# Optimization experiments

Hardware: AMD Instinct MI355X
Metric: run time of the kernel (lower is better)

The kernel has to match this reference:

```python
import jax, jax.numpy as jnp
import numpy as np

N = 50000      # nodes in batched graph
E = 800000     # edges
IN_DIM = 16
HID = 64
NH = 4         # heads
G = 128        # graphs in batch
OUT_DIM = 32
NUM_LAYERS = 8
NEG_SLOPE = 0.2  # DGL GATv2Conv default


def setup_inputs() -> dict:
    key = jax.random.key(0)
    ks = jax.random.split(key, 12)
    feat = jax.random.normal(ks[0], (N, IN_DIM), dtype=jnp.float32)
    src = jax.random.randint(ks[1], (E,), 0, N, dtype=jnp.int32)
    dst = jax.random.randint(ks[2], (E,), 0, N, dtype=jnp.int32)
    graph_ids = jnp.sort(jax.random.randint(ks[3], (N,), 0, G, dtype=jnp.int32))
    is_root = jax.random.randint(ks[4], (N,), 0, 2, dtype=jnp.int32)
    s_in = 1.0 / np.sqrt(IN_DIM)
    s_h = 1.0 / np.sqrt(2 * HID)
    s_o = 1.0 / np.sqrt(HID)
    return {
        'feat': feat, 'src': src, 'dst': dst,
        'graph_ids': graph_ids, 'is_root': is_root,
        'W_in': jax.random.normal(ks[5], (IN_DIM, HID), jnp.float32) * s_in,
        'b_in': jnp.zeros((HID,), jnp.float32),
        'W_src': jax.random.normal(ks[6], (2 * HID, NH * HID), jnp.float32) * s_h,
        'b_src': jnp.zeros((NH * HID,), jnp.float32),
        'W_dst': jax.random.normal(ks[7], (2 * HID, NH * HID), jnp.float32) * s_h,
        'b_dst': jnp.zeros((NH * HID,), jnp.float32),
        'attn': jax.random.normal(ks[8], (NH, HID), jnp.float32) * s_o,
        'W_out': jax.random.normal(ks[9], (HID, OUT_DIM), jnp.float32) * s_o,
        'b_out': jnp.zeros((OUT_DIM,), jnp.float32),
    }


def reference(feat, src, dst, graph_ids, is_root,
              W_in, b_in, W_src, b_src, W_dst, b_dst, attn, W_out, b_out):
    h0 = feat @ W_in + b_in                       # [N, HID]
    h = h0
    for _ in range(NUM_LAYERS):
        x = jnp.concatenate([h, h0], axis=1)      # [N, 2*HID]
        fs = (x @ W_src + b_src).reshape(-1, NH, HID)  # [N, NH, HID]
        fd = (x @ W_dst + b_dst).reshape(-1, NH, HID)
        # per-edge GATv2 attention logits
        e = jax.nn.leaky_relu(fs[src] + fd[dst], NEG_SLOPE)   # [E, NH, HID]
        s = jnp.einsum('ehd,hd->eh', e, attn)                 # [E, NH]
        # segment softmax over incoming edges of each dst node
        m = jax.ops.segment_max(s, dst, num_segments=N)       # [N, NH]
        a = jnp.exp(s - m[dst])
        denom = jax.ops.segment_sum(a, dst, num_segments=N)
        alpha = a / denom[dst]                                # [E, NH]
        # weighted aggregation of source features
        agg = jax.ops.segment_sum(alpha[:, :, None] * fs[src], dst,
                                  num_segments=N)             # [N, NH, HID]
        h = jnp.tanh(agg).sum(axis=1)                         # [N, HID]
    # root-weighted readout per graph
    hg = jax.ops.segment_sum(h * is_root.astype(h.dtype)[:, None],
                             graph_ids, num_segments=G)       # [G, HID]
    return hg @ W_out + b_out                                 # [G, OUT_DIM]
```

## Files before the change

kernel.cpp:

```cpp
#include <hip/hip_runtime.h>
#include <math.h>

#define N_NODES 50000
#define N_EDGES 800000
#define IN_DIM  16
#define HID     64
#define NH      4
#define NGRAPH  128
#define OUT_DIM 32
#define NUM_LAYERS 8
#define NEG_SLOPE 0.2f

#define SCAN_BLOCKS ((N_NODES + 255) / 256)

typedef unsigned short u16;
typedef unsigned char  u8;
typedef _Float16 h2   __attribute__((ext_vector_type(2)));
typedef _Float16 f16x8 __attribute__((ext_vector_type(8)));
typedef float f32x2 __attribute__((ext_vector_type(2)));
typedef __attribute__((ext_vector_type(4))) float f32x4;

static __device__ __forceinline__ u16 f2h(float f) {
    _Float16 h = (_Float16)f; u16 r; __builtin_memcpy(&r, &h, 2); return r;
}
static __device__ __forceinline__ float h2f_lo(unsigned w) {
    _Float16 h; u16 u = (u16)w; __builtin_memcpy(&h, &u, 2); return (float)h;
}
static __device__ __forceinline__ h2 shfl_h2(h2 v, int mask) {
    int i; __builtin_memcpy(&i, &v, 4); i = __shfl_xor(i, mask);
    h2 r; __builtin_memcpy(&r, &i, 4); return r;
}
static __device__ __forceinline__ h2 bcast_h2(float f) {
    _Float16 h = (_Float16)f; h2 r; r[0] = h; r[1] = h; return r;
}

#define DPP_XOR1(x) __uint_as_float((unsigned)__builtin_amdgcn_update_dpp(0, (int)__float_as_uint(x), 0xB1, 0xF, 0xF, true))
#define DPP_XOR2(x) __uint_as_float((unsigned)__builtin_amdgcn_update_dpp(0, (int)__float_as_uint(x), 0x4E, 0xF, 0xF, true))


__global__ void k_build_wpack(const float* __restrict__ Wsrc, const float* __restrict__ bsrc,
                              const float* __restrict__ Wdst, const float* __restrict__ bdst,
                              const float* __restrict__ attn,
                              u16* __restrict__ Wpack, float* __restrict__ bcat,
                              u16* __restrict__ an_h) {
    int tid = blockIdx.x * 256 + threadIdx.x;
    int i = tid & 7;
    int l = (tid >> 3) & 63;
    int rest = tid >> 9;
    int kt = rest & 3;
    int nt = rest >> 2;
    int k = kt * 32 + (l >> 4) * 8 + i;
    int col = nt * 16 + (l & 15);
    float v = (col < 256) ? Wsrc[k * 256 + col] : Wdst[k * 256 + (col - 256)];
    Wpack[tid] = f2h(v);
    if (tid < 512) bcat[tid] = (tid < 256) ? bsrc[tid] : bdst[tid - 256];
    if (tid < 256) an_h[tid] = f2h(attn[tid] * 1.44269504f);
}

__global__ void k_hist(const int* __restrict__ dst, int* __restrict__ deg) {
    int e = blockIdx.x * 256 + threadIdx.x;
    if (e < N_EDGES) atomicAdd(&deg[dst[e]], 1);
}

__global__ void k_blocksum(const int* __restrict__ deg, int* __restrict__ bsum) {
    __shared__ int sm[256];
    int i = blockIdx.x * 256 + threadIdx.x;
    sm[threadIdx.x] = (i < N_NODES) ? deg[i] : 0;
    __syncthreads();
    for (int s = 128; s > 0; s >>= 1) {
        if (threadIdx.x < s) sm[threadIdx.x] += sm[threadIdx.x + s];
        __syncthreads();
    }
    if (threadIdx.x == 0) bsum[blockIdx.x] = sm[0];
}

__global__ void k_scanbsum(int* __restrict__ bsum) {
    if (threadIdx.x == 0 && blockIdx.x == 0) {
        int acc = 0;
        for (int b = 0; b < SCAN_BLOCKS; b++) { int t = bsum[b]; bsum[b] = acc; acc += t; }
    }
}

__global__ void k_rowptr(const int* __restrict__ deg, const int* __restrict__ bsum,
                         int* __restrict__ row_ptr) {
    __shared__ int sm[256];
    int i = blockIdx.x * 256 + threadIdx.x;
    int v = (i < N_NODES) ? deg[i] : 0;
    sm[threadIdx.x] = v;
    __syncthreads();
    for (int s = 1; s < 256; s <<= 1) {
        int t = (threadIdx.x >= (unsigned)s) ? sm[threadIdx.x - s] : 0;
        __syncthreads();
        sm[threadIdx.x] += t;
        __syncthreads();
    }
    if (i < N_NODES) row_ptr[i] = bsum[blockIdx.x] + sm[threadIdx.x] - v;
}

__global__ void k_scatter(const int* __restrict__ src, const int* __restrict__ dst,
                          const int* __restrict__ row_ptr, int* __restrict__ cursor,
                          int* __restrict__ csr_src) {
    int e = blockIdx.x * 256 + threadIdx.x;
    if (e < N_EDGES) {
        int d = dst[e];
        int pos = atomicAdd(&cursor[d], 1);
        csr_src[row_ptr[d] + pos] = src[e];
    }
}

__global__ __launch_bounds__(256) void k_in_gemm(const float* __restrict__ feat,
                                                 const float* __restrict__ W,
                                                 const float* __restrict__ b,
                                                 u16* __restrict__ h0h) {
    __shared__ float sW[IN_DIM * HID];
    __shared__ float sb[HID];
    int t = threadIdx.x;
    for (int i = t; i < IN_DIM * HID; i += 256) sW[i] = W[i];
    if (t < HID) sb[t] = b[t];
    __syncthreads();
    int wid = (blockIdx.x * 256 + t) >> 6;
    int lane = t & 63;
    const float* f = feat + wid * IN_DIM;
    float acc = sb[lane];
    #pragma unroll
    for (int k = 0; k < IN_DIM; k++) acc += f[k] * sW[k * HID + lane];
    h0h[wid * HID + lane] = f2h(acc);
}


#define ST_STRIDE 152
__global__ __launch_bounds__(256) void k_gemm_mfma(const u16* __restrict__ hb,
                                                   const u16* __restrict__ h0b,
                                                   const u16* __restrict__ Wpack,
                                                   const float* __restrict__ bcat,
                                                   u16* __restrict__ fsh,
                                                   u16* __restrict__ fdh) {
    __shared__ u16 sW[16384];
    __shared__ u16 sStage[4][2432];
    int tid = threadIdx.x;
    int g  = blockIdx.x & 3;
    int tb = blockIdx.x >> 2;
    int l = tid & 63, w = tid >> 6;
    int lr = l & 15, lg = l >> 4;

    {
        const f16x8* src = (const f16x8*)(Wpack + g * 16384);
        f16x8* dst = (f16x8*)sW;
        #pragma unroll
        for (int it = 0; it < 8; it++) dst[it * 256 + tid] = src[it * 256 + tid];
    }
    __syncthreads();

    size_t row0 = (size_t)(tb * 4 + w) * 16;
    if (row0 >= N_NODES) return;

    f32x4 acc[8];
    #pragma unroll
    for (int nt = 0; nt < 8; nt++) acc[nt] = (f32x4){0.f, 0.f, 0.f, 0.f};

    #pragma unroll
    for (int kt = 0; kt < 4; kt++) {
        const u16* A = (kt < 2) ? hb : h0b;
        f16x8 a = *(const f16x8*)(A + (row0 + lr) * HID + (kt & 1) * 32 + lg * 8);
        #pragma unroll
        for (int nt = 0; nt < 8; nt++) {
            f16x8 bfr = *(const f16x8*)(sW + nt * 2048 + kt * 512 + l * 8);
            acc[nt] = __builtin_amdgcn_mfma_f32_16x16x32_f16(a, bfr, acc[nt], 0, 0, 0);
        }
    }

    u16* myst = sStage[w];
    #pragma unroll
    for (int nt = 0; nt < 8; nt++) {
        float bv = bcat[g * 128 + nt * 16 + lr];
        #pragma unroll
        for (int j = 0; j < 4; j++)
            myst[(lg * 4 + j) * ST_STRIDE + nt * 16 + lr] = f2h(acc[nt][j] + bv);
    }
    u16* dsth = (g < 2) ? fsh : fdh;
    int colh = (g & 1) * 128;
    #pragma unroll
    for (int j = 0; j < 4; j++) {
        int rloc = j * 4 + lg;
        f16x8 v = *(const f16x8*)(myst + rloc * ST_STRIDE + lr * 8);
        *(f16x8*)(dsth + (row0 + rloc) * 256 + colh + lr * 8) = v;
    }
}

__global__ __launch_bounds__(256) void k_edge(const u16* __restrict__ fsh,
                                              const u16* __restrict__ fdh,
                                              const u16* __restrict__ an_h,
                                              const int* __restrict__ row_ptr,
                                              const int* __restrict__ deg,
                                              const int* __restrict__ csr_src,
                                              u16* __restrict__ h) {
    int wid = (blockIdx.x * 256 + threadIdx.x) >> 6;
    int lane = threadIdx.x & 63;
    int g  = lane >> 4;
    int ll = lane & 15;
    const size_t ebase = (size_t)ll * 16;

    h2 an[8], fdhv[8];
    {
        const uint4* ap = (const uint4*)(an_h + ebase);
        uint4 a0 = ap[0], a1 = ap[1];
        unsigned aw[8] = {a0.x, a0.y, a0.z, a0.w, a1.x, a1.y, a1.z, a1.w};
        __builtin_memcpy(an, aw, 32);
        const uint4* fp = (const uint4*)(fdh + (size_t)wid * 256 + ebase);
        uint4 b0 = fp[0], b1 = fp[1];
        unsigned fw[8] = {b0.x, b0.y, b0.z, b0.w, b1.x, b1.y, b1.z, b1.w};
        __builtin_memcpy(fdhv, fw, 32);
    }
    const h2 slope2 = {(_Float16)NEG_SLOPE, (_Float16)NEG_SLOPE};

    float m = -3.0e38f, denom = 0.f;
    h2 agg[8];
    #pragma unroll
    for (int q = 0; q < 8; q++) agg[q] = (h2){(_Float16)0.f, (_Float16)0.f};

    int r0 = row_ptr[wid], dg = deg[wid];

    uint4 A0 = {0,0,0,0}, A1 = {0,0,0,0};
    if (g < dg) {
        int s = csr_src[r0 + g];
        const uint4* P = (const uint4*)(fsh + (size_t)s * 256 + ebase);
        A0 = P[0]; A1 = P[1];
    }

    for (int i = g; i < dg; i += 4) {
        int inext = i + 4;
        bool hN = inext < dg;
        int sN = csr_src[r0 + (hN ? inext : i)];
        const uint4* PN = (const uint4*)(fsh + (size_t)sN * 256 + ebase);
        uint4 B0 = PN[0], B1 = PN[1];

        h2 f[8];
        {
            unsigned fw[8] = {A0.x, A0.y, A0.z, A0.w, A1.x, A1.y, A1.z, A1.w};
            __builtin_memcpy(f, fw, 32);
        }
        float p0 = 0.f, p1 = 0.f;
        #pragma unroll
        for (int q = 0; q < 8; q += 2) {
            h2 e0 = f[q]   + fdhv[q];
            h2 e1 = f[q+1] + fdhv[q+1];
            h2 l0 = __builtin_elementwise_max(e0, e0 * slope2);
            h2 l1 = __builtin_elementwise_max(e1, e1 * slope2);
            p0 = __builtin_amdgcn_fdot2(l0, an[q],   p0, false);
            p1 = __builtin_amdgcn_fdot2(l1, an[q+1], p1, false);
        }
        float p = p0 + p1;
        p += DPP_XOR1(p);
        p += DPP_XOR2(p);

        float c;
        if (__builtin_expect(p > m + 4.f, 0)) {
            float rs = exp2f(m - p);
            h2 rs2 = bcast_h2(rs);
            #pragma unroll
            for (int q = 0; q < 8; q++) agg[q] = agg[q] * rs2;
            denom *= rs;
            m = p;
            c = 1.f;
        } else {
            c = exp2f(p - m);
        }
        h2 c2 = bcast_h2(c);
        #pragma unroll
        for (int q = 0; q < 8; q++) agg[q] = agg[q] + f[q] * c2;
        denom += c;

        A0 = B0; A1 = B1;
    }

    {
        float mm = fmaxf(m, __shfl_xor(m, 16));
        mm = fmaxf(mm, __shfl_xor(mm, 32));
        float sc = exp2f(m - mm);
        denom *= sc;
        h2 sc2 = bcast_h2(sc);
        #pragma unroll
        for (int q = 0; q < 8; q++) agg[q] = agg[q] * sc2;
        denom += __shfl_xor(denom, 16);
        denom += __shfl_xor(denom, 32);
        #pragma unroll
        for (int q = 0; q < 8; q++) {
            agg[q] = agg[q] + shfl_h2(agg[q], 16);
            agg[q] = agg[q] + shfl_h2(agg[q], 32);
        }
    }

    float inv = denom > 0.f ? __builtin_amdgcn_rcpf(denom) : 0.f;
    float inv2 = inv * 2.885390082f;

    h2 x0 = (g & 2) ? ((g & 1) ? agg[6] : agg[4]) : ((g & 1) ? agg[2] : agg[0]);
    h2 x1 = (g & 2) ? ((g & 1) ? agg[7] : agg[5]) : ((g & 1) ? agg[3] : agg[1]);
    float t[4] = {(float)x0[0], (float)x0[1], (float)x1[0], (float)x1[1]};
    #pragma unroll
    for (int j = 0; j < 4; j++) {
        float E = exp2f(t[j] * inv2);
        float r = __builtin_amdgcn_rcpf(E + 1.f);
        float v = fmaf(-2.f, r, 1.f);
        v += __shfl_xor(v, 4);
        v += __shfl_xor(v, 8);
        t[j] = v;
    }
    if (ll < 4) {
        uint2 o;
        o.x = (unsigned)f2h(t[0]) | ((unsigned)f2h(t[1]) << 16);
        o.y = (unsigned)f2h(t[2]) | ((unsigned)f2h(t[3]) << 16);
        *(uint2*)(h + (size_t)wid * 64 + ll * 16 + g * 4) = o;
    }
}


__global__ __launch_bounds__(256) void k_readout(const u16* __restrict__ h,
                                                 const int* __restrict__ graph_ids,
                                                 const int* __restrict__ is_root,
                                                 float* __restrict__ hg) {
    int wid = (blockIdx.x * 256 + threadIdx.x) >> 6;
    int lane = threadIdx.x & 63;
    if (is_root[wid]) {
        int g = graph_ids[wid];
        atomicAdd(&hg[g * HID + lane], h2f_lo(h[(size_t)wid * HID + lane]));
    }
}

__global__ void k_out_gemm(const float* __restrict__ hg, const float* __restrict__ W,
                           const float* __restrict__ b, float* __restrict__ out) {
    int i = blockIdx.x * 256 + threadIdx.x;
    if (i >= NGRAPH * OUT_DIM) return;
    int g = i >> 5, o = i & 31;
    float acc = b[o];
    #pragma unroll
    for (int k = 0; k < HID; k++) acc += hg[g * HID + k] * W[k * OUT_DIM + o];
    out[i] = acc;
}


extern "C" void kernel_launch(void* const* d_in, const int* in_sizes, int n_in,
                              void* d_out, int out_size, void* d_ws, size_t ws_size,
                              hipStream_t stream) {
    const float* feat      = (const float*)d_in[0];
    const int*   src       = (const int*)d_in[1];
    const int*   dst       = (const int*)d_in[2];
    const int*   graph_ids = (const int*)d_in[3];
    const int*   is_root   = (const int*)d_in[4];
    const float* W_in      = (const float*)d_in[5];
    const float* b_in      = (const float*)d_in[6];
    const float* W_src     = (const float*)d_in[7];
    const float* b_src     = (const float*)d_in[8];
    const float* W_dst     = (const float*)d_in[9];
    const float* b_dst     = (const float*)d_in[10];
    const float* attn      = (const float*)d_in[11];
    const float* W_out     = (const float*)d_in[12];
    const float* b_out     = (const float*)d_in[13];
    float* out = (float*)d_out;

    char* base = (char*)d_ws;
    size_t off = 0;
    auto carve = [&](size_t bytes) -> char* {
        char* p = base + off;
        off = (off + bytes + 255) & ~(size_t)255;
        return p;
    };
    u16*   h0b     = (u16*)carve((size_t)N_NODES * HID * 2);
    u16*   hb      = (u16*)carve((size_t)N_NODES * HID * 2);
    u16*   fsh     = (u16*)carve((size_t)N_NODES * 256 * 2);
    u16*   fdh     = (u16*)carve((size_t)N_NODES * 256 * 2);
    u16*   Wpack   = (u16*)carve(128 * 512 * 2);
    float* bcat    = (float*)carve(512 * 4);
    u16*   an_h    = (u16*)carve(256 * 2);
    int*   csr_src = (int*)carve((size_t)N_EDGES * 4);
    int*   row_ptr = (int*)carve((size_t)N_NODES * 4);
    int*   bsum    = (int*)carve(SCAN_BLOCKS * 4);
    char*  zero0   = carve(0);
    int*   deg     = (int*)carve((size_t)N_NODES * 4);
    int*   cursor  = (int*)carve((size_t)N_NODES * 4);
    float* hg      = (float*)carve((size_t)NGRAPH * HID * 4);
    char*  zero1   = base + off;
    if (off > ws_size) return;

    (void)hipMemsetAsync(zero0, 0, (size_t)(zero1 - zero0), stream);

    k_build_wpack<<<256, 256, 0, stream>>>(W_src, b_src, W_dst, b_dst, attn, Wpack, bcat, an_h);
    k_hist<<<(N_EDGES + 255) / 256, 256, 0, stream>>>(dst, deg);
    k_blocksum<<<SCAN_BLOCKS, 256, 0, stream>>>(deg, bsum);
    k_scanbsum<<<1, 64, 0, stream>>>(bsum);
    k_rowptr<<<SCAN_BLOCKS, 256, 0, stream>>>(deg, bsum, row_ptr);
    k_scatter<<<(N_EDGES + 255) / 256, 256, 0, stream>>>(src, dst, row_ptr, cursor, csr_src);

    k_in_gemm<<<N_NODES / 4, 256, 0, stream>>>(feat, W_in, b_in, h0b);

    const int gemm_grid = ((N_NODES / 16 + 3) / 4) * 4;
    for (int layer = 0; layer < NUM_LAYERS; layer++) {
        const u16* hcur = (layer == 0) ? h0b : hb;
        k_gemm_mfma<<<gemm_grid, 256, 0, stream>>>(hcur, h0b, Wpack, bcat, fsh, fdh);
        k_edge<<<N_NODES / 4, 256, 0, stream>>>(fsh, fdh, an_h, row_ptr, deg, csr_src, hb);
    }

    k_readout<<<N_NODES / 4, 256, 0, stream>>>(hb, graph_ids, is_root, hg);
    k_out_gemm<<<(NGRAPH * OUT_DIM + 255) / 256, 256, 0, stream>>>(hg, W_out, b_out, out);
}
```

Before: 862.7 us.

## Fuse all stages into one persistent cooperative kernel with grid syncs

```diff
diff --git a/kernel.cpp b/kernel.cpp
--- a/kernel.cpp
+++ b/kernel.cpp
@@ -1,5 +1,8 @@
 #include <hip/hip_runtime.h>
+#include <hip/hip_cooperative_groups.h>
 #include <math.h>
+
+namespace cg = cooperative_groups;
 
 #define N_NODES 50000
 #define N_EDGES 800000
@@ -12,12 +15,11 @@
 #define NEG_SLOPE 0.2f
 
 #define SCAN_BLOCKS ((N_NODES + 255) / 256)
+#define ST_STRIDE 152
 
 typedef unsigned short u16;
-typedef unsigned char  u8;
 typedef _Float16 h2   __attribute__((ext_vector_type(2)));
 typedef _Float16 f16x8 __attribute__((ext_vector_type(8)));
-typedef float f32x2 __attribute__((ext_vector_type(2)));
 typedef __attribute__((ext_vector_type(4))) float f32x4;
 
 static __device__ __forceinline__ u16 f2h(float f) {
@@ -37,325 +39,294 @@
 #define DPP_XOR1(x) __uint_as_float((unsigned)__builtin_amdgcn_update_dpp(0, (int)__float_as_uint(x), 0xB1, 0xF, 0xF, true))
 #define DPP_XOR2(x) __uint_as_float((unsigned)__builtin_amdgcn_update_dpp(0, (int)__float_as_uint(x), 0x4E, 0xF, 0xF, true))
 
-
-__global__ void k_build_wpack(const float* __restrict__ Wsrc, const float* __restrict__ bsrc,
-                              const float* __restrict__ Wdst, const float* __restrict__ bdst,
-                              const float* __restrict__ attn,
-                              u16* __restrict__ Wpack, float* __restrict__ bcat,
-                              u16* __restrict__ an_h) {
-    int tid = blockIdx.x * 256 + threadIdx.x;
-    int i = tid & 7;
-    int l = (tid >> 3) & 63;
-    int rest = tid >> 9;
-    int kt = rest & 3;
-    int nt = rest >> 2;
-    int k = kt * 32 + (l >> 4) * 8 + i;
-    int col = nt * 16 + (l & 15);
-    float v = (col < 256) ? Wsrc[k * 256 + col] : Wdst[k * 256 + (col - 256)];
-    Wpack[tid] = f2h(v);
-    if (tid < 512) bcat[tid] = (tid < 256) ? bsrc[tid] : bdst[tid - 256];
-    if (tid < 256) an_h[tid] = f2h(attn[tid] * 1.44269504f);
-}
-
-__global__ void k_hist(const int* __restrict__ dst, int* __restrict__ deg) {
-    int e = blockIdx.x * 256 + threadIdx.x;
-    if (e < N_EDGES) atomicAdd(&deg[dst[e]], 1);
-}
-
-__global__ void k_blocksum(const int* __restrict__ deg, int* __restrict__ bsum) {
-    __shared__ int sm[256];
-    int i = blockIdx.x * 256 + threadIdx.x;
-    sm[threadIdx.x] = (i < N_NODES) ? deg[i] : 0;
+struct Params {
+    const float* feat; const int* src; const int* dst;
+    const int* graph_ids; const int* is_root;
+    const float* W_in; const float* b_in;
+    const float* W_src; const float* b_src;
+    const float* W_dst; const float* b_dst;
+    const float* attn; const float* W_out; const float* b_out;
+    float* out;
+    u16* h0b; u16* hb; u16* fsh; u16* fdh; u16* Wpack;
+    float* bcat; u16* an_h;
+    int* csr_src; int* row_ptr; int* bsum; int* deg; int* cursor;
+    float* hg;
+};
+
+__global__ __launch_bounds__(256, 4) void k_fused(Params P) {
+    cg::grid_group grid = cg::this_grid();
+    const int bid = blockIdx.x, nb = gridDim.x, tid = threadIdx.x;
+    const int gthread = bid * 256 + tid, nthreads = nb * 256;
+    const int l = tid & 63, w = tid >> 6;
+    const int lr = l & 15, lg = l >> 4;
+
+    __shared__ __align__(16) char smem_raw[19456];
+
+    for (int i = gthread; i < N_NODES; i += nthreads) { P.deg[i] = 0; P.cursor[i] = 0; }
+    for (int i = gthread; i < NGRAPH * HID; i += nthreads) P.hg[i] = 0.f;
+    for (int t = gthread; t < 65536; t += nthreads) {
+        int ii = t & 7;
+        int ll2 = (t >> 3) & 63;
+        int rest = t >> 9;
+        int kt = rest & 3;
+        int nt = rest >> 2;
+        int k = kt * 32 + (ll2 >> 4) * 8 + ii;
+        int col = nt * 16 + (ll2 & 15);
+        float v = (col < 256) ? P.W_src[k * 256 + col] : P.W_dst[k * 256 + (col - 256)];
+        P.Wpack[t] = f2h(v);
+        if (t < 512) P.bcat[t] = (t < 256) ? P.b_src[t] : P.b_dst[t - 256];
+        if (t < 256) P.an_h[t] = f2h(P.attn[t] * 1.44269504f);
+    }
+    grid.sync();
+
+    for (int e = gthread; e < N_EDGES; e += nthreads) atomicAdd(&P.deg[P.dst[e]], 1);
+    grid.sync();
+
+    int* sm = (int*)smem_raw;
+    if (bid < SCAN_BLOCKS) {
+        int i = bid * 256 + tid;
+        sm[tid] = (i < N_NODES) ? P.deg[i] : 0;
+        __syncthreads();
+        for (int s = 128; s > 0; s >>= 1) {
+            if (tid < s) sm[tid] += sm[tid + s];
+            __syncthreads();
+        }
+        if (tid == 0) P.bsum[bid] = sm[0];
+    }
+    grid.sync();
+
+    if (bid == 0 && tid == 0) {
+        int acc = 0;
+        for (int b = 0; b < SCAN_BLOCKS; b++) { int t2 = P.bsum[b]; P.bsum[b] = acc; acc += t2; }
+    }
+    grid.sync();
+
+    if (bid < SCAN_BLOCKS) {
+        int i = bid * 256 + tid;
+        int v = (i < N_NODES) ? P.deg[i] : 0;
+        sm[tid] = v;
+        __syncthreads();
+        for (int s = 1; s < 256; s <<= 1) {
+            int t2 = (tid >= s) ? sm[tid - s] : 0;
+            __syncthreads();
+            sm[tid] += t2;
+            __syncthreads();
+        }
+        if (i < N_NODES) P.row_ptr[i] = P.bsum[bid] + sm[tid] - v;
+    }
+    grid.sync();
+
+    for (int e = gthread; e < N_EDGES; e += nthreads) {
+        int d = P.dst[e];
+        int pos = atomicAdd(&P.cursor[d], 1);
+        P.csr_src[P.row_ptr[d] + pos] = P.src[e];
+    }
     __syncthreads();
-    for (int s = 128; s > 0; s >>= 1) {
-        if (threadIdx.x < s) sm[threadIdx.x] += sm[threadIdx.x + s];
-        __syncthreads();
-    }
-    if (threadIdx.x == 0) bsum[blockIdx.x] = sm[0];
-}
-
-__global__ void k_scanbsum(int* __restrict__ bsum) {
-    if (threadIdx.x == 0 && blockIdx.x == 0) {
-        int acc = 0;
-        for (int b = 0; b < SCAN_BLOCKS; b++) { int t = bsum[b]; bsum[b] = acc; acc += t; }
-    }
-}
-
-__global__ void k_rowptr(const int* __restrict__ deg, const int* __restrict__ bsum,
-                         int* __restrict__ row_ptr) {
-    __shared__ int sm[256];
-    int i = blockIdx.x * 256 + threadIdx.x;
-    int v = (i < N_NODES) ? deg[i] : 0;
-    sm[threadIdx.x] = v;
+    float* sWin = (float*)smem_raw;
+    float* sbin = sWin + 1024;
+    for (int i = tid; i < IN_DIM * HID; i += 256) sWin[i] = P.W_in[i];
+    if (tid < HID) sbin[tid] = P.b_in[tid];
     __syncthreads();
-    for (int s = 1; s < 256; s <<= 1) {
-        int t = (threadIdx.x >= (unsigned)s) ? sm[threadIdx.x - s] : 0;
-        __syncthreads();
-        sm[threadIdx.x] += t;
-        __syncthreads();
-    }
-    if (i < N_NODES) row_ptr[i] = bsum[blockIdx.x] + sm[threadIdx.x] - v;
-}
-
-__global__ void k_scatter(const int* __restrict__ src, const int* __restrict__ dst,
-                          const int* __restrict__ row_ptr, int* __restrict__ cursor,
-                          int* __restrict__ csr_src) {
-    int e = blockIdx.x * 256 + threadIdx.x;
-    if (e < N_EDGES) {
-        int d = dst[e];
-        int pos = atomicAdd(&cursor[d], 1);
-        csr_src[row_ptr[d] + pos] = src[e];
-    }
-}
-
-__global__ __launch_bounds__(256) void k_in_gemm(const float* __restrict__ feat,
-                                                 const float* __restrict__ W,
-                                                 const float* __restrict__ b,
-                                                 u16* __restrict__ h0h) {
-    __shared__ float sW[IN_DIM * HID];
-    __shared__ float sb[HID];
-    int t = threadIdx.x;
-    for (int i = t; i < IN_DIM * HID; i += 256) sW[i] = W[i];
-    if (t < HID) sb[t] = b[t];
-    __syncthreads();
-    int wid = (blockIdx.x * 256 + t) >> 6;
-    int lane = t & 63;
-    const float* f = feat + wid * IN_DIM;
-    float acc = sb[lane];
-    #pragma unroll
-    for (int k = 0; k < IN_DIM; k++) acc += f[k] * sW[k * HID + lane];
-    h0h[wid * HID + lane] = f2h(acc);
-}
-
-
-#define ST_STRIDE 152
-__global__ __launch_bounds__(256) void k_gemm_mfma(const u16* __restrict__ hb,
-                                                   const u16* __restrict__ h0b,
-                                                   const u16* __restrict__ Wpack,
-                                                   const float* __restrict__ bcat,
-                                                   u16* __restrict__ fsh,
-                                                   u16* __restrict__ fdh) {
-    __shared__ u16 sW[16384];
-    __shared__ u16 sStage[4][2432];
-    int tid = threadIdx.x;
-    int g  = blockIdx.x & 3;
-    int tb = blockIdx.x >> 2;
-    int l = tid & 63, w = tid >> 6;
-    int lr = l & 15, lg = l >> 4;
-
-    {
-        const f16x8* src = (const f16x8*)(Wpack + g * 16384);
-        f16x8* dst = (f16x8*)sW;
+    for (int v = bid; v < N_NODES / 4; v += nb) {
+        int node = v * 4 + w;
+        const float* f = P.feat + node * IN_DIM;
+        float acc = sbin[l];
         #pragma unroll
-        for (int it = 0; it < 8; it++) dst[it * 256 + tid] = src[it * 256 + tid];
-    }
-    __syncthreads();
-
-    size_t row0 = (size_t)(tb * 4 + w) * 16;
-    if (row0 >= N_NODES) return;
-
-    f32x4 acc[8];
-    #pragma unroll
-    for (int nt = 0; nt < 8; nt++) acc[nt] = (f32x4){0.f, 0.f, 0.f, 0.f};
-
-    #pragma unroll
-    for (int kt = 0; kt < 4; kt++) {
-        const u16* A = (kt < 2) ? hb : h0b;
-        f16x8 a = *(const f16x8*)(A + (row0 + lr) * HID + (kt & 1) * 32 + lg * 8);
+        for (int k = 0; k < IN_DIM; k++) acc += f[k] * sWin[k * HID + l];
+        P.h0b[node * HID + l] = f2h(acc);
+    }
+    grid.sync();
+
+    const int nbg = nb >> 2;
+    const int g = bid & 3;
+    const int myg = bid >> 2;
+    const u16* WpG = P.Wpack + g * 16384;
+    u16* sStage = (u16*)smem_raw;
+    const h2 slope2 = {(_Float16)NEG_SLOPE, (_Float16)NEG_SLOPE};
+
+    for (int layer = 0; layer < NUM_LAYERS; layer++) {
+        const u16* hcur = (layer == 0) ? P.h0b : P.hb;
+
+        for (int tb = myg; tb < (N_NODES / 16 + 3) / 4; tb += nbg) {
+            size_t row0 = (size_t)(tb * 4 + w) * 16;
+            if (row0 >= N_NODES) continue;
+            f32x4 acc[8];
+            #pragma unroll
+            for (int nt = 0; nt < 8; nt++) acc[nt] = (f32x4){0.f, 0.f, 0.f, 0.f};
+            #pragma unroll
+            for (int kt = 0; kt < 4; kt++) {
+                const u16* A = (kt < 2) ? hcur : P.h0b;
+                f16x8 a = *(const f16x8*)(A + (row0 + lr) * HID + (kt & 1) * 32 + lg * 8);
+                #pragma unroll
+                for (int nt = 0; nt < 8; nt++) {
+                    f16x8 bfr = *(const f16x8*)(WpG + nt * 2048 + kt * 512 + l * 8);
+                    acc[nt] = __builtin_amdgcn_mfma_f32_16x16x32_f16(a, bfr, acc[nt], 0, 0, 0);
+                }
+            }
+            u16* myst = sStage + w * 2432;
+            #pragma unroll
+            for (int nt = 0; nt < 8; nt++) {
+                float bv = P.bcat[g * 128 + nt * 16 + lr];
+                #pragma unroll
+                for (int j = 0; j < 4; j++)
+                    myst[(lg * 4 + j) * ST_STRIDE + nt * 16 + lr] = f2h(acc[nt][j] + bv);
+            }
+            u16* dsth = (g < 2) ? P.fsh : P.fdh;
+            int colh = (g & 1) * 128;
+            #pragma unroll
+            for (int j = 0; j < 4; j++) {
+                int rloc = j * 4 + lg;
+                f16x8 vv = *(const f16x8*)(myst + rloc * ST_STRIDE + lr * 8);
+                *(f16x8*)(dsth + (row0 + rloc) * 256 + colh + lr * 8) = vv;
+            }
+        }
+        grid.sync();
+
+        for (int v = bid; v < N_NODES / 4; v += nb) {
+            int wid = v * 4 + w;
+            int eg = lg;
+            int ll = lr;
+            const size_t ebase = (size_t)ll * 16;
+
+            h2 an[8], fdhv[8];
+            {
+                const uint4* ap = (const uint4*)(P.an_h + ebase);
+                uint4 a0 = ap[0], a1 = ap[1];
+                unsigned aw[8] = {a0.x, a0.y, a0.z, a0.w, a1.x, a1.y, a1.z, a1.w};
+                __builtin_memcpy(an, aw, 32);
+                const uint4* fp = (const uint4*)(P.fdh + (size_t)wid * 256 + ebase);
+                uint4 b0 = fp[0], b1 = fp[1];
+                unsigned fw[8] = {b0.x, b0.y, b0.z, b0.w, b1.x, b1.y, b1.z, b1.w};
+                __builtin_memcpy(fdhv, fw, 32);
+            }
+
+            float m = -3.0e38f, denom = 0.f;
+            h2 agg[8];
+            #pragma unroll
+            for (int q = 0; q < 8; q++) agg[q] = (h2){(_Float16)0.f, (_Float16)0.f};
+
+            int r0 = P.row_ptr[wid], dg = P.deg[wid];
+            for (int i = eg; i < dg; i += 4) {
+                int s = P.csr_src[r0 + i];
+                const uint4* Pr = (const uint4*)(P.fsh + (size_t)s * 256 + ebase);
+                uint4 A0 = Pr[0], A1 = Pr[1];
+                h2 f[8];
+                {
+                    unsigned fw[8] = {A0.x, A0.y, A0.z, A0.w, A1.x, A1.y, A1.z, A1.w};
+                    __builtin_memcpy(f, fw, 32);
+                }
+                float p0 = 0.f, p1 = 0.f;
+                #pragma unroll
+                for (int q = 0; q < 8; q += 2) {
+                    h2 e0 = f[q]   + fdhv[q];
+                    h2 e1 = f[q+1] + fdhv[q+1];
+                    h2 l0 = __builtin_elementwise_max(e0, e0 * slope2);
+                    h2 l1 = __builtin_elementwise_max(e1, e1 * slope2);
+                    p0 = __builtin_amdgcn_fdot2(l0, an[q],   p0, false);
+                    p1 = __builtin_amdgcn_fdot2(l1, an[q+1], p1, false);
+                }
+                float p = p0 + p1;
+                p += DPP_XOR1(p);
+                p += DPP_XOR2(p);
+
+                float c;
+                if (__builtin_expect(p > m + 4.f, 0)) {
+                    float rs = exp2f(m - p);
+                    h2 rs2 = bcast_h2(rs);
+                    #pragma unroll
+                    for (int q = 0; q < 8; q++) agg[q] = agg[q] * rs2;
+                    denom *= rs;
+                    m = p;
+                    c = 1.f;
+                } else {
+                    c = exp2f(p - m);
+                }
+                h2 c2 = bcast_h2(c);
+                #pragma unroll
+                for (int q = 0; q < 8; q++) agg[q] = agg[q] + f[q] * c2;
+                denom += c;
+            }
+
+            {
+                float mm = fmaxf(m, __shfl_xor(m, 16));
+                mm = fmaxf(mm, __shfl_xor(mm, 32));
+                float sc = exp2f(m - mm);
+                denom *= sc;
+                h2 sc2 = bcast_h2(sc);
+                #pragma unroll
+                for (int q = 0; q < 8; q++) agg[q] = agg[q] * sc2;
+                denom += __shfl_xor(denom, 16);
+                denom += __shfl_xor(denom, 32);
+                #pragma unroll
+                for (int q = 0; q < 8; q++) {
+                    agg[q] = agg[q] + shfl_h2(agg[q], 16);
+                    agg[q] = agg[q] + shfl_h2(agg[q], 32);
+                }
+            }
+
+            float inv = denom > 0.f ? __builtin_amdgcn_rcpf(denom) : 0.f;
+            float inv2 = inv * 2.885390082f;
+
+            h2 x0 = (eg & 2) ? ((eg & 1) ? agg[6] : agg[4]) : ((eg & 1) ? agg[2] : agg[0]);
+            h2 x1 = (eg & 2) ? ((eg & 1) ? agg[7] : agg[5]) : ((eg & 1) ? agg[3] : agg[1]);
+            float t[4] = {(float)x0[0], (float)x0[1], (float)x1[0], (float)x1[1]};
+            #pragma unroll
+            for (int j = 0; j < 4; j++) {
+                float E = exp2f(t[j] * inv2);
+                float r = __builtin_amdgcn_rcpf(E + 1.f);
+                float vv = fmaf(-2.f, r, 1.f);
+                vv += __shfl_xor(vv, 4);
+                vv += __shfl_xor(vv, 8);
+                t[j] = vv;
+            }
+            if (ll < 4) {
+                uint2 o;
+                o.x = (unsigned)f2h(t[0]) | ((unsigned)f2h(t[1]) << 16);
+                o.y = (unsigned)f2h(t[2]) | ((unsigned)f2h(t[3]) << 16);
+                *(uint2*)(P.hb + (size_t)wid * 64 + ll * 16 + eg * 4) = o;
+            }
+        }
+        grid.sync();
+    }
+
+    for (int v = bid; v < N_NODES / 4; v += nb) {
+        int wid = v * 4 + w;
+        if (P.is_root[wid]) {
+            int gg = P.graph_ids[wid];
+            atomicAdd(&P.hg[gg * HID + l], h2f_lo(P.hb[(size_t)wid * HID + l]));
+        }
+    }
+    grid.sync();
+
+    for (int i = gthread; i < NGRAPH * OUT_DIM; i += nthreads) {
+        int gg = i >> 5, o = i & 31;
+        float acc = P.b_out[o];
         #pragma unroll
-        for (int nt = 0; nt < 8; nt++) {
-            f16x8 bfr = *(const f16x8*)(sW + nt * 2048 + kt * 512 + l * 8);
-            acc[nt] = __builtin_amdgcn_mfma_f32_16x16x32_f16(a, bfr, acc[nt], 0, 0, 0);
-        }
-    }
-
-    u16* myst = sStage[w];
-    #pragma unroll
-    for (int nt = 0; nt < 8; nt++) {
-        float bv = bcat[g * 128 + nt * 16 + lr];
-        #pragma unroll
-        for (int j = 0; j < 4; j++)
-            myst[(lg * 4 + j) * ST_STRIDE + nt * 16 + lr] = f2h(acc[nt][j] + bv);
-    }
-    u16* dsth = (g < 2) ? fsh : fdh;
-    int colh = (g & 1) * 128;
-    #pragma unroll
-    for (int j = 0; j < 4; j++) {
-        int rloc = j * 4 + lg;
-        f16x8 v = *(const f16x8*)(myst + rloc * ST_STRIDE + lr * 8);
-        *(f16x8*)(dsth + (row0 + rloc) * 256 + colh + lr * 8) = v;
-    }
-}
-
-__global__ __launch_bounds__(256) void k_edge(const u16* __restrict__ fsh,
-                                              const u16* __restrict__ fdh,
-                                              const u16* __restrict__ an_h,
-                                              const int* __restrict__ row_ptr,
-                                              const int* __restrict__ deg,
-                                              const int* __restrict__ csr_src,
-                                              u16* __restrict__ h) {
-    int wid = (blockIdx.x * 256 + threadIdx.x) >> 6;
-    int lane = threadIdx.x & 63;
-    int g  = lane >> 4;
-    int ll = lane & 15;
-    const size_t ebase = (size_t)ll * 16;
-
-    h2 an[8], fdhv[8];
-    {
-        const uint4* ap = (const uint4*)(an_h + ebase);
-        uint4 a0 = ap[0], a1 = ap[1];
-        unsigned aw[8] = {a0.x, a0.y, a0.z, a0.w, a1.x, a1.y, a1.z, a1.w};
-        __builtin_memcpy(an, aw, 32);
-        const uint4* fp = (const uint4*)(fdh + (size_t)wid * 256 + ebase);
-        uint4 b0 = fp[0], b1 = fp[1];
-        unsigned fw[8] = {b0.x, b0.y, b0.z, b0.w, b1.x, b1.y, b1.z, b1.w};
-        __builtin_memcpy(fdhv, fw, 32);
-    }
-    const h2 slope2 = {(_Float16)NEG_SLOPE, (_Float16)NEG_SLOPE};
-
-    float m = -3.0e38f, denom = 0.f;
-    h2 agg[8];
-    #pragma unroll
-    for (int q = 0; q < 8; q++) agg[q] = (h2){(_Float16)0.f, (_Float16)0.f};
-
-    int r0 = row_ptr[wid], dg = deg[wid];
-
-    uint4 A0 = {0,0,0,0}, A1 = {0,0,0,0};
-    if (g < dg) {
-        int s = csr_src[r0 + g];
-        const uint4* P = (const uint4*)(fsh + (size_t)s * 256 + ebase);
-        A0 = P[0]; A1 = P[1];
-    }
-
-    for (int i = g; i < dg; i += 4) {
-        int inext = i + 4;
-        bool hN = inext < dg;
-        int sN = csr_src[r0 + (hN ? inext : i)];
-        const uint4* PN = (const uint4*)(fsh + (size_t)sN * 256 + ebase);
-        uint4 B0 = PN[0], B1 = PN[1];
-
-        h2 f[8];
-        {
-            unsigned fw[8] = {A0.x, A0.y, A0.z, A0.w, A1.x, A1.y, A1.z, A1.w};
-            __builtin_memcpy(f, fw, 32);
-        }
-        float p0 = 0.f, p1 = 0.f;
-        #pragma unroll
-        for (int q = 0; q < 8; q += 2) {
-            h2 e0 = f[q]   + fdhv[q];
-            h2 e1 = f[q+1] + fdhv[q+1];
-            h2 l0 = __builtin_elementwise_max(e0, e0 * slope2);
-            h2 l1 = __builtin_elementwise_max(e1, e1 * slope2);
-            p0 = __builtin_amdgcn_fdot2(l0, an[q],   p0, false);
-            p1 = __builtin_amdgcn_fdot2(l1, an[q+1], p1, false);
-        }
-        float p = p0 + p1;
-        p += DPP_XOR1(p);
-        p += DPP_XOR2(p);
-
-        float c;
-        if (__builtin_expect(p > m + 4.f, 0)) {
-            float rs = exp2f(m - p);
-            h2 rs2 = bcast_h2(rs);
-            #pragma unroll
-            for (int q = 0; q < 8; q++) agg[q] = agg[q] * rs2;
-            denom *= rs;
-            m = p;
-            c = 1.f;
-        } else {
-            c = exp2f(p - m);
-        }
-        h2 c2 = bcast_h2(c);
-        #pragma unroll
-        for (int q = 0; q < 8; q++) agg[q] = agg[q] + f[q] * c2;
-        denom += c;
-
-        A0 = B0; A1 = B1;
-    }
-
-    {
-        float mm = fmaxf(m, __shfl_xor(m, 16));
-        mm = fmaxf(mm, __shfl_xor(mm, 32));
-        float sc = exp2f(m - mm);
-        denom *= sc;
-        h2 sc2 = bcast_h2(sc);
-        #pragma unroll
-        for (int q = 0; q < 8; q++) agg[q] = agg[q] * sc2;
-        denom += __shfl_xor(denom, 16);
-        denom += __shfl_xor(denom, 32);
-        #pragma unroll
-        for (int q = 0; q < 8; q++) {
-            agg[q] = agg[q] + shfl_h2(agg[q], 16);
-            agg[q] = agg[q] + shfl_h2(agg[q], 32);
-        }
-    }
-
-    float inv = denom > 0.f ? __builtin_amdgcn_rcpf(denom) : 0.f;
-    float inv2 = inv * 2.885390082f;
-
-    h2 x0 = (g & 2) ? ((g & 1) ? agg[6] : agg[4]) : ((g & 1) ? agg[2] : agg[0]);
-    h2 x1 = (g & 2) ? ((g & 1) ? agg[7] : agg[5]) : ((g & 1) ? agg[3] : agg[1]);
-    float t[4] = {(float)x0[0], (float)x0[1], (float)x1[0], (float)x1[1]};
-    #pragma unroll
-    for (int j = 0; j < 4; j++) {
-        float E = exp2f(t[j] * inv2);
-        float r = __builtin_amdgcn_rcpf(E + 1.f);
-        float v = fmaf(-2.f, r, 1.f);
-        v += __shfl_xor(v, 4);
-        v += __shfl_xor(v, 8);
-        t[j] = v;
-    }
-    if (ll < 4) {
-        uint2 o;
-        o.x = (unsigned)f2h(t[0]) | ((unsigned)f2h(t[1]) << 16);
-        o.y = (unsigned)f2h(t[2]) | ((unsigned)f2h(t[3]) << 16);
-        *(uint2*)(h + (size_t)wid * 64 + ll * 16 + g * 4) = o;
-    }
-}
-
-
-__global__ __launch_bounds__(256) void k_readout(const u16* __restrict__ h,
-                                                 const int* __restrict__ graph_ids,
-                                                 const int* __restrict__ is_root,
-                                                 float* __restrict__ hg) {
-    int wid = (blockIdx.x * 256 + threadIdx.x) >> 6;
-    int lane = threadIdx.x & 63;
-    if (is_root[wid]) {
-        int g = graph_ids[wid];
-        atomicAdd(&hg[g * HID + lane], h2f_lo(h[(size_t)wid * HID + lane]));
-    }
-}
-
-__global__ void k_out_gemm(const float* __restrict__ hg, const float* __restrict__ W,
-                           const float* __restrict__ b, float* __restrict__ out) {
-    int i = blockIdx.x * 256 + threadIdx.x;
-    if (i >= NGRAPH * OUT_DIM) return;
-    int g = i >> 5, o = i & 31;
-    float acc = b[o];
-    #pragma unroll
-    for (int k = 0; k < HID; k++) acc += hg[g * HID + k] * W[k * OUT_DIM + o];
-    out[i] = acc;
+        for (int k = 0; k < HID; k++) acc += P.hg[gg * HID + k] * P.W_out[k * OUT_DIM + o];
+        P.out[i] = acc;
+    }
 }
 
 
 extern "C" void kernel_launch(void* const* d_in, const int* in_sizes, int n_in,
                               void* d_out, int out_size, void* d_ws, size_t ws_size,
                               hipStream_t stream) {
-    const float* feat      = (const float*)d_in[0];
-    const int*   src       = (const int*)d_in[1];
-    const int*   dst       = (const int*)d_in[2];
-    const int*   graph_ids = (const int*)d_in[3];
-    const int*   is_root   = (const int*)d_in[4];
-    const float* W_in      = (const float*)d_in[5];
-    const float* b_in      = (const float*)d_in[6];
-    const float* W_src     = (const float*)d_in[7];
-    const float* b_src     = (const float*)d_in[8];
-    const float* W_dst     = (const float*)d_in[9];
-    const float* b_dst     = (const float*)d_in[10];
-    const float* attn      = (const float*)d_in[11];
-    const float* W_out     = (const float*)d_in[12];
-    const float* b_out     = (const float*)d_in[13];
-    float* out = (float*)d_out;
+    Params P;
+    P.feat      = (const float*)d_in[0];
+    P.src       = (const int*)d_in[1];
+    P.dst       = (const int*)d_in[2];
+    P.graph_ids = (const int*)d_in[3];
+    P.is_root   = (const int*)d_in[4];
+    P.W_in      = (const float*)d_in[5];
+    P.b_in      = (const float*)d_in[6];
+    P.W_src     = (const float*)d_in[7];
+    P.b_src     = (const float*)d_in[8];
+    P.W_dst     = (const float*)d_in[9];
+    P.b_dst     = (const float*)d_in[10];
+    P.attn      = (const float*)d_in[11];
+    P.W_out     = (const float*)d_in[12];
+    P.b_out     = (const float*)d_in[13];
+    P.out       = (float*)d_out;
 
     char* base = (char*)d_ws;
     size_t off = 0;
@@ -364,41 +335,29 @@
         off = (off + bytes + 255) & ~(size_t)255;
         return p;
     };
-    u16*   h0b     = (u16*)carve((size_t)N_NODES * HID * 2);
-    u16*   hb      = (u16*)carve((size_t)N_NODES * HID * 2);
-    u16*   fsh     = (u16*)carve((size_t)N_NODES * 256 * 2);
-    u16*   fdh     = (u16*)carve((size_t)N_NODES * 256 * 2);
-    u16*   Wpack   = (u16*)carve(128 * 512 * 2);
-    float* bcat    = (float*)carve(512 * 4);
-    u16*   an_h    = (u16*)carve(256 * 2);
-    int*   csr_src = (int*)carve((size_t)N_EDGES * 4);
-    int*   row_ptr = (int*)carve((size_t)N_NODES * 4);
-    int*   bsum    = (int*)carve(SCAN_BLOCKS * 4);
-    char*  zero0   = carve(0);
-    int*   deg     = (int*)carve((size_t)N_NODES * 4);
-    int*   cursor  = (int*)carve((size_t)N_NODES * 4);
-    float* hg      = (float*)carve((size_t)NGRAPH * HID * 4);
-    char*  zero1   = base + off;
+    P.h0b     = (u16*)carve((size_t)N_NODES * HID * 2);
+    P.hb      = (u16*)carve((size_t)N_NODES * HID * 2);
+    P.fsh     = (u16*)carve((size_t)N_NODES * 256 * 2);
+    P.fdh     = (u16*)carve((size_t)N_NODES * 256 * 2);
+    P.Wpack   = (u16*)carve(128 * 512 * 2);
+    P.bcat    = (float*)carve(512 * 4);
+    P.an_h    = (u16*)carve(256 * 2);
+    P.csr_src = (int*)carve((size_t)N_EDGES * 4);
+    P.row_ptr = (int*)carve((size_t)N_NODES * 4);
+    P.bsum    = (int*)carve(SCAN_BLOCKS * 4);
+    P.deg     = (int*)carve((size_t)N_NODES * 4);
+    P.cursor  = (int*)carve((size_t)N_NODES * 4);
+    P.hg      = (float*)carve((size_t)NGRAPH * HID * 4);
     if (off > ws_size) return;
 
-    (void)hipMemsetAsync(zero0, 0, (size_t)(zero1 - zero0), stream);
-
-    k_build_wpack<<<256, 256, 0, stream>>>(W_src, b_src, W_dst, b_dst, attn, Wpack, bcat, an_h);
-    k_hist<<<(N_EDGES + 255) / 256, 256, 0, stream>>>(dst, deg);
-    k_blocksum<<<SCAN_BLOCKS, 256, 0, stream>>>(deg, bsum);
-    k_scanbsum<<<1, 64, 0, stream>>>(bsum);
-    k_rowptr<<<SCAN_BLOCKS, 256, 0, stream>>>(deg, bsum, row_ptr);
-    k_scatter<<<(N_EDGES + 255) / 256, 256, 0, stream>>>(src, dst, row_ptr, cursor, csr_src);
-
-    k_in_gemm<<<N_NODES / 4, 256, 0, stream>>>(feat, W_in, b_in, h0b);
-
-    const int gemm_grid = ((N_NODES / 16 + 3) / 4) * 4;
-    for (int layer = 0; layer < NUM_LAYERS; layer++) {
-        const u16* hcur = (layer == 0) ? h0b : hb;
-        k_gemm_mfma<<<gemm_grid, 256, 0, stream>>>(hcur, h0b, Wpack, bcat, fsh, fdh);
-        k_edge<<<N_NODES / 4, 256, 0, stream>>>(fsh, fdh, an_h, row_ptr, deg, csr_src, hb);
-    }
-
-    k_readout<<<N_NODES / 4, 256, 0, stream>>>(hb, graph_ids, is_root, hg);
-    k_out_gemm<<<(NGRAPH * OUT_DIM + 255) / 256, 256, 0, stream>>>(hg, W_out, b_out, out);
-}
+    int maxb = 0;
+    (void)hipOccupancyMaxActiveBlocksPerMultiprocessor(&maxb, k_fused, 256, 0);
+    if (maxb < 1) maxb = 1;
+    long long cap = (long long)maxb * 256;
+    int grid = (cap > 1024) ? 1024 : (int)cap;
+    grid &= ~3;
+    if (grid < 256) grid = 256;
+
+    void* args[] = { &P };
+    (void)hipLaunchCooperativeKernel(k_fused, dim3(grid), dim3(256), args, 0, stream);
+}
```

Result: slower. 2.924 ms (+238.9%).
